# Kernel tuning notes

Hardware: AMD Instinct MI355X
Metric: run time of the kernel (lower is better)

The kernel has to match this reference:

```python
import jax, jax.numpy as jnp
import numpy as np

RATIO_THRESHOLD = 0.8  # Lowe ratio
DISTANCE_THRESHOLD = None
DO_MUTUAL_CHECK = True


def setup_inputs() -> dict:
    key = jax.random.key(0)
    k0, k1 = jax.random.split(key)
    b, d, n, m = 8, 256, 4096, 4096
    d0 = jax.random.normal(k0, (b, d, n), dtype=jnp.float32)
    d1 = jax.random.normal(k1, (b, d, m), dtype=jnp.float32)
    # L2-normalize along descriptor dim so sim is cosine similarity in [-1, 1]
    d0 = d0 / jnp.linalg.norm(d0, axis=1, keepdims=True)
    d1 = d1 / jnp.linalg.norm(d1, axis=1, keepdims=True)
    return {"descriptors0": d0, "descriptors1": d1}


def find_nn(sim, ratio_thresh, distance_thresh):
    k = 2 if ratio_thresh else 1
    sim_nn, ind_nn = jax.lax.top_k(sim, k)  # [b, n, k]
    dist_nn = 2.0 * (1.0 - sim_nn)
    mask = jnp.ones(ind_nn.shape[:-1], dtype=bool)
    if ratio_thresh:
        mask = mask & (dist_nn[..., 0] <= (ratio_thresh ** 2) * dist_nn[..., 1])
    if distance_thresh:
        mask = mask & (dist_nn[..., 0] <= distance_thresh ** 2)
    matches = jnp.where(mask, ind_nn[..., 0], -1)
    scores = jnp.where(mask, (sim_nn[..., 0] + 1.0) / 2.0, 0.0)
    return matches, scores


def mutual_check(m0, m1):
    inds0 = jnp.arange(m0.shape[-1])
    safe = jnp.where(m0 > -1, m0, 0)
    loop = jnp.take_along_axis(m1, safe, axis=-1)
    ok = (m0 > -1) & (inds0 == loop)
    return jnp.where(ok, m0, -1)


def reference(descriptors0, descriptors1):
    # sim[b, n, m] = <desc0[:, :, n], desc1[:, :, m]>
    sim = jnp.einsum("bdn,bdm->bnm", descriptors0, descriptors1)
    matches0, scores0 = find_nn(sim, RATIO_THRESHOLD, DISTANCE_THRESHOLD)
    if DO_MUTUAL_CHECK:
        matches1, _ = find_nn(jnp.swapaxes(sim, 1, 2), RATIO_THRESHOLD, DISTANCE_THRESHOLD)
        matches0 = mutual_check(matches0, matches1)
    return matches0, scores0
```

## Files before the change

kernel.cpp:

```cpp
#include <hip/hip_runtime.h>


typedef unsigned int uint;
typedef unsigned char uchar;
typedef int i32x4 __attribute__((ext_vector_type(4)));
typedef int i32x8 __attribute__((ext_vector_type(8)));
typedef float f32x4 __attribute__((ext_vector_type(4)));

constexpr int B_ = 8, D_ = 256, N_ = 4096;
constexpr int BMR = 128;
constexpr int BNT = 128;
constexpr int CSPLIT = 2;
constexpr int MT_ITERS = (N_ / CSPLIT) / BNT;


constexpr size_t SZ_PANEL = (size_t)B_ * N_ * D_;
constexpr size_t OFF_AT = 0;
constexpr size_t OFF_BT = SZ_PANEL;
constexpr size_t OFF_PR = 2 * SZ_PANEL;
constexpr size_t SZ_PR  = (size_t)4 * B_ * N_ * 8;
constexpr size_t OFF_PC = OFF_PR + SZ_PR;

__device__ __forceinline__ uchar f2e4m3(float f) {
  uint u = __float_as_uint(f);
  uint s = (u >> 24) & 0x80u;
  uint mag = u & 0x7FFFFFFFu;
  if (mag >= 0x43E00000u) return (uchar)(s | 0x7Eu);
  int e = (int)(mag >> 23) - 127;
  if (e >= -6) {
    uint m = (mag >> 20) & 7u;
    uint rem = mag & 0xFFFFFu;
    m += (rem > 0x80000u) || (rem == 0x80000u && (m & 1u));
    uint ef = (uint)(e + 7);
    if (m == 8u) { m = 0u; ef += 1u; }
    if (ef >= 16u) return (uchar)(s | 0x7Eu);
    return (uchar)(s | (ef << 3) | m);
  } else {
    int q = __float2int_rn(__uint_as_float(mag) * 512.0f);
    if (q >= 8) return (uchar)(s | 0x08u);
    return (uchar)(s | (uint)q);
  }
}

__device__ __forceinline__ void glds16(const void* g, void* l) {
  __builtin_amdgcn_global_load_lds(
      (const __attribute__((address_space(1))) void*)(uintptr_t)(g),
      (__attribute__((address_space(3))) void*)(uint32_t)(uintptr_t)(l),
      16, 0, 0);
}

__device__ __forceinline__ float packkey(float v, uint mask, uint tag) {
  return __uint_as_float((__float_as_uint(v) & mask) | tag);
}

__device__ __forceinline__ float med3f(float a, float b, float c) {
#if __has_builtin(__builtin_amdgcn_fmed3f)
  return __builtin_amdgcn_fmed3f(a, b, c);
#else
  return fmaxf(fminf(a, b), fminf(fmaxf(a, b), c));
#endif
}

__device__ __forceinline__ void top2p(float& s1, float& s2, float k0, float k1) {
  const float mid = med3f(s1, k0, k1);
  s1 = fmaxf(fmaxf(s1, k0), k1);
  s2 = fmaxf(s2, mid);
}

__device__ __forceinline__ void top2merge(float& s1, float& s2, float o1, float o2) {
  const float lo = fminf(s1, o1);
  s1 = fmaxf(s1, o1);
  s2 = fmaxf(lo, fmaxf(s2, o2));
}

__global__ __launch_bounds__(256)
void prep_kernel(const float* __restrict__ in0, const float* __restrict__ in1,
                 uchar* __restrict__ At, uchar* __restrict__ Bt)
{
  __shared__ uchar tile[128][44];
  const int bz = blockIdx.z;
  const float* src = (bz < 8) ? in0 : in1;
  uchar* dst = (bz < 8) ? At : Bt;
  const int b = bz & 7;
  const int n0 = blockIdx.x * 128;
  const int k0b = blockIdx.y * 32;
  const int t = threadIdx.x;

  const int kq = t >> 5;
  const int n4 = (t & 31) * 4;
  const float* pin = src + ((size_t)b * D_ + k0b + kq * 4) * N_ + n0 + n4;
  float4 v[4];
  #pragma unroll
  for (int j = 0; j < 4; ++j) v[j] = *(const float4*)(pin + (size_t)j * N_);
  #pragma unroll
  for (int i = 0; i < 4; ++i) {
    uchar4 o = make_uchar4(f2e4m3(((const float*)&v[0])[i]),
                           f2e4m3(((const float*)&v[1])[i]),
                           f2e4m3(((const float*)&v[2])[i]),
                           f2e4m3(((const float*)&v[3])[i]));
    *(uchar4*)&tile[n4 + i][kq * 4] = o;
  }
  __syncthreads();

  const int nl = t & 127, h = t >> 7;
  const int kg = k0b + h * 16;
  const int ks = kg >> 7, g = (kg >> 5) & 3, hh = (kg >> 4) & 1;
  const int q = (nl >> 6) & 1, r4 = (nl >> 4) & 3, i16 = nl & 15;
  i32x4 val;
  #pragma unroll
  for (int j = 0; j < 4; ++j)
    val[j] = *(const int*)&tile[nl][h * 16 + j * 4];
  uchar* po = dst + (size_t)b * (N_ * D_) + (size_t)blockIdx.x * 32768 +
              ks * 16384 + ((q * 4 + r4) * 2 + hh) * 1024 + (g * 16 + i16) * 16;
  *(i32x4*)po = val;
}

__global__ __launch_bounds__(256, 2)
void nn_pass(const uchar* __restrict__ A, const uchar* __restrict__ Bp,
             uint2* __restrict__ partR, uint2* __restrict__ partC)
{
  __shared__ uchar Bs[2][32768];

  const int t = threadIdx.x;
  const int bid = blockIdx.x;
  const int b = bid & 7;
  const int rb = (bid >> 3) & 31;
  const int cs = bid >> 8;
  const size_t bOff = (size_t)b * (N_ * D_);
  const int r0 = rb * BMR;

  const int l = t & 63, wid = t >> 6, wm = wid >> 1, wn = wid & 1;
  const int l15 = l & 15, g = l >> 4;
  const int lds0 = t * 16;

  const uchar* Aseg = A + bOff + (size_t)rb * 32768;
  const uchar* Bb = Bp + bOff + (size_t)cs * 524288;

  #pragma unroll
  for (int i = 0; i < 8; ++i)
    glds16(Bb + i * 4096 + lds0, (char*)Bs[0] + i * 4096 + lds0);

  i32x8 af[2][4];
  #pragma unroll
  for (int ks = 0; ks < 2; ++ks)
    #pragma unroll
    for (int mi = 0; mi < 4; ++mi) {
      const uchar* p = Aseg + ks * 16384 + ((wm * 4 + mi) * 2) * 1024 + l * 16;
      const i32x4 lo = *(const i32x4*)p;
      const i32x4 hi = *(const i32x4*)(p + 1024);
      af[ks][mi] = __builtin_shufflevector(lo, hi, 0, 1, 2, 3, 4, 5, 6, 7);
    }
  __syncthreads();

  const float NEG = __uint_as_float(0xFF800000u);
  float rs1[4][4], rs2[4][4];
  #pragma unroll
  for (int mi = 0; mi < 4; ++mi)
    #pragma unroll
    for (int rg = 0; rg < 4; ++rg) { rs1[mi][rg] = NEG; rs2[mi][rg] = NEG; }

  float cp1[4], cp2[4];

  #pragma unroll 1
  for (int mt = 0; mt < MT_ITERS; ++mt) {
    const char* cB = (const char*)Bs[mt & 1] + l * 16;

    if (mt + 1 < MT_ITERS) {
      const uchar* Bnx = Bb + (size_t)(mt + 1) * 32768;
      #pragma unroll
      for (int i = 0; i < 8; ++i)
        glds16(Bnx + i * 4096 + lds0, (char*)Bs[(mt + 1) & 1] + i * 4096 + lds0);
    }

    if (mt > 0 && g == 0) {
      const int cbp = (mt - 1) * BNT + wn * 64;
      #pragma unroll
      for (int ni = 0; ni < 4; ++ni)
        partC[((size_t)(rb * 2 + wm) * B_ + b) * N_ + cs * 2048 + cbp + ni * 16 + l15] =
            make_uint2(__float_as_uint(cp1[ni]), __float_as_uint(cp2[ni]));
    }

    f32x4 acc[4][4];
    #pragma unroll
    for (int mi = 0; mi < 4; ++mi)
      #pragma unroll
      for (int ni = 0; ni < 4; ++ni) acc[mi][ni] = (f32x4){0.f, 0.f, 0.f, 0.f};

    #pragma unroll
    for (int ni = 0; ni < 4; ++ni) {
      const int imm = ((wn * 4 + ni) * 2) * 1024;
      const i32x4 lo = *(const i32x4*)(cB + imm);
      const i32x4 hi = *(const i32x4*)(cB + imm + 1024);
      const i32x8 bf = __builtin_shufflevector(lo, hi, 0, 1, 2, 3, 4, 5, 6, 7);
      __builtin_amdgcn_s_setprio(1);
      #pragma unroll
      for (int mi = 0; mi < 4; ++mi)
        acc[mi][ni] = __builtin_amdgcn_mfma_scale_f32_16x16x128_f8f6f4(
            af[0][mi], bf, acc[mi][ni], 0, 0, 0, 127, 0, 127);
      __builtin_amdgcn_s_setprio(0);
    }
    #pragma unroll
    for (int ni = 0; ni < 4; ++ni) {
      const int imm = 16384 + ((wn * 4 + ni) * 2) * 1024;
      const i32x4 lo = *(const i32x4*)(cB + imm);
      const i32x4 hi = *(const i32x4*)(cB + imm + 1024);
      const i32x8 bf = __builtin_shufflevector(lo, hi, 0, 1, 2, 3, 4, 5, 6, 7);
      __builtin_amdgcn_s_setprio(1);
      #pragma unroll
      for (int mi = 0; mi < 4; ++mi)
        acc[mi][ni] = __builtin_amdgcn_mfma_scale_f32_16x16x128_f8f6f4(
            af[1][mi], bf, acc[mi][ni], 0, 0, 0, 127, 0, 127);
      __builtin_amdgcn_s_setprio(0);
    }

    const int colb = mt * BNT + wn * 64;
    const uint tg0 = (uint)(2047 - (colb + l15));
    #pragma unroll
    for (int mi = 0; mi < 4; ++mi)
      #pragma unroll
      for (int rg = 0; rg < 4; ++rg) {
        const float k0 = packkey(acc[mi][0][rg], 0xFFFFF800u, tg0);
        const float k1 = packkey(acc[mi][1][rg], 0xFFFFF800u, tg0 - 16);
        const float k2 = packkey(acc[mi][2][rg], 0xFFFFF800u, tg0 - 32);
        const float k3 = packkey(acc[mi][3][rg], 0xFFFFF800u, tg0 - 48);
        top2p(rs1[mi][rg], rs2[mi][rg], k0, k1);
        top2p(rs1[mi][rg], rs2[mi][rg], k2, k3);
      }
    const uint tgb = (uint)(63 - g * 4);
    #pragma unroll
    for (int ni = 0; ni < 4; ++ni) {
      float c1 = NEG, c2 = NEG;
      #pragma unroll
      for (int mi = 0; mi < 4; ++mi) {
        const float k0 = packkey(acc[mi][ni][0], 0xFFFFFFC0u, tgb - (uint)(mi * 16));
        const float k1 = packkey(acc[mi][ni][1], 0xFFFFFFC0u, tgb - (uint)(mi * 16 + 1));
        const float k2 = packkey(acc[mi][ni][2], 0xFFFFFFC0u, tgb - (uint)(mi * 16 + 2));
        const float k3 = packkey(acc[mi][ni][3], 0xFFFFFFC0u, tgb - (uint)(mi * 16 + 3));
        top2p(c1, c2, k0, k1);
        top2p(c1, c2, k2, k3);
      }
      #pragma unroll
      for (int off = 16; off <= 32; off <<= 1) {
        const float o1 = __shfl_xor(c1, off);
        const float o2 = __shfl_xor(c2, off);
        top2merge(c1, c2, o1, o2);
      }
      cp1[ni] = c1; cp2[ni] = c2;
    }
    __syncthreads();
  }

  if (g == 0) {
    const int cbp = (MT_ITERS - 1) * BNT + wn * 64;
    #pragma unroll
    for (int ni = 0; ni < 4; ++ni)
      partC[((size_t)(rb * 2 + wm) * B_ + b) * N_ + cs * 2048 + cbp + ni * 16 + l15] =
          make_uint2(__float_as_uint(cp1[ni]), __float_as_uint(cp2[ni]));
  }

  #pragma unroll
  for (int off = 1; off < 16; off <<= 1) {
    #pragma unroll
    for (int mi = 0; mi < 4; ++mi)
      #pragma unroll
      for (int rg = 0; rg < 4; ++rg) {
        const float o1 = __shfl_xor(rs1[mi][rg], off);
        const float o2 = __shfl_xor(rs2[mi][rg], off);
        top2merge(rs1[mi][rg], rs2[mi][rg], o1, o2);
      }
  }
  if (l15 == 0) {
    #pragma unroll
    for (int mi = 0; mi < 4; ++mi)
      #pragma unroll
      for (int rg = 0; rg < 4; ++rg)
        partR[((size_t)(cs * 2 + wn) * B_ + b) * N_ + r0 + wm * 64 + mi * 16 + g * 4 + rg] =
            make_uint2(__float_as_uint(rs1[mi][rg]), __float_as_uint(rs2[mi][rg]));
  }
}

__global__ __launch_bounds__(256)
void finalize_kernel(const uint2* __restrict__ pR, const uint2* __restrict__ pC,
                     float* __restrict__ out)
{
  const int i = blockIdx.x * 256 + threadIdx.x;
  if (i >= B_ * N_) return;
  const int b = i >> 12;
  const int n = i & (N_ - 1);
  const float NEG = __uint_as_float(0xFF800000u);

  float s1 = NEG, s2 = NEG; int bs = 0;
  #pragma unroll
  for (int sl = 0; sl < 4; ++sl) {
    const uint2 v = pR[(size_t)sl * B_ * N_ + i];
    const float o1 = __uint_as_float(v.x), o2 = __uint_as_float(v.y);
    bs = (o1 > s1) ? sl : bs;
    top2merge(s1, s2, o1, o2);
  }
  const uint k1 = __float_as_uint(s1);
  const int col = (bs >> 1) * 2048 + 2047 - (int)(k1 & 0x7FFu);
  const float v1 = __uint_as_float(k1 & 0xFFFFF800u);
  const float v2 = __uint_as_float(__float_as_uint(s2) & 0xFFFFF800u);
  const bool ok = (1.0f - v1) <= 0.64f * (1.0f - v2);

  out[B_ * N_ + i] = ok ? (v1 + 1.0f) * 0.5f : 0.0f;

  int res = -1;
  if (ok) {
    float c1 = NEG, c2 = NEG; int cbs = 0;
    const uint2* pcb = pC + (size_t)b * N_ + col;
    #pragma unroll 8
    for (int sl = 0; sl < 64; ++sl) {
      const uint2 v = pcb[(size_t)sl * B_ * N_];
      const float o1 = __uint_as_float(v.x), o2 = __uint_as_float(v.y);
      cbs = (o1 > c1) ? sl : cbs;
      top2merge(c1, c2, o1, o2);
    }
    const uint ck1 = __float_as_uint(c1);
    const int row = cbs * 64 + 63 - (int)(ck1 & 0x3Fu);
    const float cv1 = __uint_as_float(ck1 & 0xFFFFFFC0u);
    const float cv2 = __uint_as_float(__float_as_uint(c2) & 0xFFFFFFC0u);
    const bool cok = (1.0f - cv1) <= 0.64f * (1.0f - cv2);
    if (cok && row == n) res = col;
  }
  out[i] = (float)res;
}

extern "C" void kernel_launch(void* const* d_in, const int* in_sizes, int n_in,
                              void* d_out, int out_size, void* d_ws, size_t ws_size,
                              hipStream_t stream)
{
  const float* d0 = (const float*)d_in[0];
  const float* d1 = (const float*)d_in[1];
  float* out = (float*)d_out;

  uchar* At = (uchar*)((char*)d_ws + OFF_AT);
  uchar* Bt = (uchar*)((char*)d_ws + OFF_BT);
  uint2* PR = (uint2*)((char*)d_ws + OFF_PR);
  uint2* PC = (uint2*)((char*)d_ws + OFF_PC);

  prep_kernel<<<dim3(N_ / 128, D_ / 32, 16), 256, 0, stream>>>(d0, d1, At, Bt);
  nn_pass<<<dim3(B_ * (N_ / BMR) * CSPLIT), 256, 0, stream>>>(At, Bt, PR, PC);
  finalize_kernel<<<dim3(B_ * N_ / 256), 256, 0, stream>>>(PR, PC, out);
}
```

Measured before the change: 77.34 us.

## Stage B tiles through a three-slot half-tile LDS ring and buffer column partials

Replaces the two-slot, full-tile LDS double buffer with a three-slot ring of half-tiles, one per K-slice. Loads are issued further ahead, with explicit vmcnt waits and raw s_barrier calls placed between compute phases. Column top-2 partials now go to an LDS scratch buffer instead of being stored to global memory inside the main loop, and are written out with coalesced stores at the end. This aims to keep global stores out of the vmcnt accounting and to overlap B loads with MFMA work more smoothly. The cost is more LDS per block, which could limit occupancy, and four barriers per iteration instead of one.

```diff
diff --git a/kernel.cpp b/kernel.cpp
--- a/kernel.cpp
+++ b/kernel.cpp
@@ -73,6 +73,9 @@
   s2 = fmaxf(lo, fmaxf(s2, o2));
 }
 
+#define CFENCE() asm volatile("" ::: "memory")
+#define BARRIER() do { CFENCE(); __builtin_amdgcn_s_barrier(); CFENCE(); } while (0)
+
 __global__ __launch_bounds__(256)
 void prep_kernel(const float* __restrict__ in0, const float* __restrict__ in1,
                  uchar* __restrict__ At, uchar* __restrict__ Bt)
@@ -119,7 +122,8 @@
 void nn_pass(const uchar* __restrict__ A, const uchar* __restrict__ Bp,
              uint2* __restrict__ partR, uint2* __restrict__ partC)
 {
-  __shared__ uchar Bs[2][32768];
+  __shared__ uchar ring[3][16384];
+  __shared__ uint2 scrC[4096];
 
   const int t = threadIdx.x;
   const int bid = blockIdx.x;
@@ -136,10 +140,6 @@
   const uchar* Aseg = A + bOff + (size_t)rb * 32768;
   const uchar* Bb = Bp + bOff + (size_t)cs * 524288;
 
-  #pragma unroll
-  for (int i = 0; i < 8; ++i)
-    glds16(Bb + i * 4096 + lds0, (char*)Bs[0] + i * 4096 + lds0);
-
   i32x8 af[2][4];
   #pragma unroll
   for (int ks = 0; ks < 2; ++ks)
@@ -150,42 +150,17 @@
       const i32x4 hi = *(const i32x4*)(p + 1024);
       af[ks][mi] = __builtin_shufflevector(lo, hi, 0, 1, 2, 3, 4, 5, 6, 7);
     }
-  __syncthreads();
-
-  const float NEG = __uint_as_float(0xFF800000u);
-  float rs1[4][4], rs2[4][4];
-  #pragma unroll
-  for (int mi = 0; mi < 4; ++mi)
-    #pragma unroll
-    for (int rg = 0; rg < 4; ++rg) { rs1[mi][rg] = NEG; rs2[mi][rg] = NEG; }
-
-  float cp1[4], cp2[4];
-
-  #pragma unroll 1
-  for (int mt = 0; mt < MT_ITERS; ++mt) {
-    const char* cB = (const char*)Bs[mt & 1] + l * 16;
-
-    if (mt + 1 < MT_ITERS) {
-      const uchar* Bnx = Bb + (size_t)(mt + 1) * 32768;
-      #pragma unroll
-      for (int i = 0; i < 8; ++i)
-        glds16(Bnx + i * 4096 + lds0, (char*)Bs[(mt + 1) & 1] + i * 4096 + lds0);
-    }
-
-    if (mt > 0 && g == 0) {
-      const int cbp = (mt - 1) * BNT + wn * 64;
-      #pragma unroll
-      for (int ni = 0; ni < 4; ++ni)
-        partC[((size_t)(rb * 2 + wm) * B_ + b) * N_ + cs * 2048 + cbp + ni * 16 + l15] =
-            make_uint2(__float_as_uint(cp1[ni]), __float_as_uint(cp2[ni]));
-    }
-
-    f32x4 acc[4][4];
-    #pragma unroll
-    for (int mi = 0; mi < 4; ++mi)
-      #pragma unroll
-      for (int ni = 0; ni < 4; ++ni) acc[mi][ni] = (f32x4){0.f, 0.f, 0.f, 0.f};
-
+
+  auto STAGE = [&](int tile, int ksl, int slot) {
+    const uchar* src = Bb + (size_t)tile * 32768 + (size_t)ksl * 16384;
+    char* dst = (char*)ring[slot];
+    #pragma unroll
+    for (int i = 0; i < 4; ++i)
+      glds16(src + i * 4096 + lds0, dst + i * 4096 + lds0);
+  };
+
+  auto COMPUTE = [&](int slot, const i32x8 (&afk)[4], f32x4 (&acc)[4][4]) {
+    const char* cB = (const char*)ring[slot] + l * 16;
     #pragma unroll
     for (int ni = 0; ni < 4; ++ni) {
       const int imm = ((wn * 4 + ni) * 2) * 1024;
@@ -196,23 +171,19 @@
       #pragma unroll
       for (int mi = 0; mi < 4; ++mi)
         acc[mi][ni] = __builtin_amdgcn_mfma_scale_f32_16x16x128_f8f6f4(
-            af[0][mi], bf, acc[mi][ni], 0, 0, 0, 127, 0, 127);
+            afk[mi], bf, acc[mi][ni], 0, 0, 0, 127, 0, 127);
       __builtin_amdgcn_s_setprio(0);
     }
-    #pragma unroll
-    for (int ni = 0; ni < 4; ++ni) {
-      const int imm = 16384 + ((wn * 4 + ni) * 2) * 1024;
-      const i32x4 lo = *(const i32x4*)(cB + imm);
-      const i32x4 hi = *(const i32x4*)(cB + imm + 1024);
-      const i32x8 bf = __builtin_shufflevector(lo, hi, 0, 1, 2, 3, 4, 5, 6, 7);
-      __builtin_amdgcn_s_setprio(1);
-      #pragma unroll
-      for (int mi = 0; mi < 4; ++mi)
-        acc[mi][ni] = __builtin_amdgcn_mfma_scale_f32_16x16x128_f8f6f4(
-            af[1][mi], bf, acc[mi][ni], 0, 0, 0, 127, 0, 127);
-      __builtin_amdgcn_s_setprio(0);
-    }
-
+  };
+
+  const float NEG = __uint_as_float(0xFF800000u);
+  float rs1[4][4], rs2[4][4];
+  #pragma unroll
+  for (int mi = 0; mi < 4; ++mi)
+    #pragma unroll
+    for (int rg = 0; rg < 4; ++rg) { rs1[mi][rg] = NEG; rs2[mi][rg] = NEG; }
+
+  auto FOLD = [&](int mt, f32x4 (&acc)[4][4]) {
     const int colb = mt * BNT + wn * 64;
     const uint tg0 = (uint)(2047 - (colb + l15));
     #pragma unroll
@@ -245,17 +216,74 @@
         const float o2 = __shfl_xor(c2, off);
         top2merge(c1, c2, o1, o2);
       }
-      cp1[ni] = c1; cp2[ni] = c2;
+      if (g == 0)
+        scrC[(((mt * 2 + wm) * 2 + wn) * 4 + ni) * 16 + l15] =
+            make_uint2(__float_as_uint(c1), __float_as_uint(c2));
     }
-    __syncthreads();
-  }
-
-  if (g == 0) {
-    const int cbp = (MT_ITERS - 1) * BNT + wn * 64;
-    #pragma unroll
-    for (int ni = 0; ni < 4; ++ni)
-      partC[((size_t)(rb * 2 + wm) * B_ + b) * N_ + cs * 2048 + cbp + ni * 16 + l15] =
-          make_uint2(__float_as_uint(cp1[ni]), __float_as_uint(cp2[ni]));
+  };
+
+  STAGE(0, 0, 0);
+  STAGE(0, 1, 1);
+  asm volatile("s_waitcnt vmcnt(0)" ::: "memory");
+  BARRIER();
+
+  int rcur = 0;
+
+  #pragma unroll 1
+  for (int mt = 0; mt < MT_ITERS - 1; ++mt) {
+    f32x4 acc[4][4];
+    #pragma unroll
+    for (int mi = 0; mi < 4; ++mi)
+      #pragma unroll
+      for (int ni = 0; ni < 4; ++ni) acc[mi][ni] = (f32x4){0.f, 0.f, 0.f, 0.f};
+
+    int rn2 = rcur + 2; if (rn2 >= 3) rn2 -= 3;
+    int rn1 = rcur + 1; if (rn1 >= 3) rn1 -= 3;
+
+    STAGE(mt + 1, 0, rn2);
+    asm volatile("s_waitcnt vmcnt(8)" ::: "memory");
+    BARRIER();
+    COMPUTE(rcur, af[0], acc);
+    BARRIER();
+
+    STAGE(mt + 1, 1, rcur);
+    asm volatile("s_waitcnt vmcnt(8)" ::: "memory");
+    BARRIER();
+    COMPUTE(rn1, af[1], acc);
+    FOLD(mt, acc);
+    BARRIER();
+
+    rcur = rn2;
+  }
+
+  {
+    f32x4 acc[4][4];
+    #pragma unroll
+    for (int mi = 0; mi < 4; ++mi)
+      #pragma unroll
+      for (int ni = 0; ni < 4; ++ni) acc[mi][ni] = (f32x4){0.f, 0.f, 0.f, 0.f};
+    int rn1 = rcur + 1; if (rn1 >= 3) rn1 -= 3;
+
+    asm volatile("s_waitcnt vmcnt(4)" ::: "memory");
+    BARRIER();
+    COMPUTE(rcur, af[0], acc);
+    BARRIER();
+
+    asm volatile("s_waitcnt vmcnt(0)" ::: "memory");
+    BARRIER();
+    COMPUTE(rn1, af[1], acc);
+    FOLD(MT_ITERS - 1, acc);
+    BARRIER();
+  }
+
+  {
+    const int wmD = t >> 7;
+    const int cc = t & 127;
+    const uint2* sp = &scrC[(size_t)(((cc >> 3) * 2 + wmD) * 2 + ((cc >> 2) & 1)) * 64 +
+                            (cc & 3) * 16];
+    uint2* gp = partC + ((size_t)(rb * 2 + wmD) * B_ + b) * N_ + cs * 2048 + cc * 16;
+    #pragma unroll
+    for (int j = 0; j < 16; ++j) gp[j] = sp[j];
   }
 
   #pragma unroll
```

Result: no change. 77.61 us (+0.4%).

## Retile NN pass to 64-row blocks with 8 column waves and split-K staging

Applied to the files above, without the earlier changes.

Reorganizes the fused GEMM+top2 kernel: blocks now cover 64 rows with 512 threads, each of 8 waves owning a 16-column slice, and the B tile is staged in two K-halves so the next half's load overlaps the current MFMAs. Per-wave accumulators shrink from 16 to 4 vectors, cutting register pressure to allow higher occupancy, and LDS per block is halved. In exchange, A fragments are loaded twice as often across blocks, the block count doubles, there are more barriers per iteration, and partR grows to 16 slices that finalize must merge.

```diff
diff --git a/kernel.cpp b/kernel.cpp
--- a/kernel.cpp
+++ b/kernel.cpp
@@ -8,17 +8,15 @@
 typedef float f32x4 __attribute__((ext_vector_type(4)));
 
 constexpr int B_ = 8, D_ = 256, N_ = 4096;
-constexpr int BMR = 128;
-constexpr int BNT = 128;
 constexpr int CSPLIT = 2;
-constexpr int MT_ITERS = (N_ / CSPLIT) / BNT;
+constexpr int MT_ITERS = (N_ / CSPLIT) / 128;
 
 
 constexpr size_t SZ_PANEL = (size_t)B_ * N_ * D_;
 constexpr size_t OFF_AT = 0;
 constexpr size_t OFF_BT = SZ_PANEL;
 constexpr size_t OFF_PR = 2 * SZ_PANEL;
-constexpr size_t SZ_PR  = (size_t)4 * B_ * N_ * 8;
+constexpr size_t SZ_PR  = (size_t)16 * B_ * N_ * 8;
 constexpr size_t OFF_PC = OFF_PR + SZ_PR;
 
 __device__ __forceinline__ uchar f2e4m3(float f) {
@@ -61,6 +59,12 @@
 #endif
 }
 
+__device__ __forceinline__ void top2(float& s1, float& s2, float k) {
+  const float m = med3f(s1, s2, k);
+  s1 = fmaxf(s1, k);
+  s2 = m;
+}
+
 __device__ __forceinline__ void top2p(float& s1, float& s2, float k0, float k1) {
   const float mid = med3f(s1, k0, k1);
   s1 = fmaxf(fmaxf(s1, k0), k1);
@@ -115,37 +119,42 @@
   *(i32x4*)po = val;
 }
 
-__global__ __launch_bounds__(256, 2)
+__global__ __launch_bounds__(512, 4)
 void nn_pass(const uchar* __restrict__ A, const uchar* __restrict__ Bp,
              uint2* __restrict__ partR, uint2* __restrict__ partC)
 {
-  __shared__ uchar Bs[2][32768];
+  __shared__ uchar Bs[2][16384];
 
   const int t = threadIdx.x;
   const int bid = blockIdx.x;
   const int b = bid & 7;
-  const int rb = (bid >> 3) & 31;
-  const int cs = bid >> 8;
+  const int rb = (bid >> 3) & 63;
+  const int cs = bid >> 9;
   const size_t bOff = (size_t)b * (N_ * D_);
-  const int r0 = rb * BMR;
-
-  const int l = t & 63, wid = t >> 6, wm = wid >> 1, wn = wid & 1;
+  const int r0 = rb * 64;
+
+  const int l = t & 63, wn = t >> 6;
   const int l15 = l & 15, g = l >> 4;
   const int lds0 = t * 16;
 
-  const uchar* Aseg = A + bOff + (size_t)rb * 32768;
+  const uchar* Apan = A + bOff + (size_t)(rb >> 1) * 32768;
+  const int q = rb & 1;
   const uchar* Bb = Bp + bOff + (size_t)cs * 524288;
 
-  #pragma unroll
-  for (int i = 0; i < 8; ++i)
-    glds16(Bb + i * 4096 + lds0, (char*)Bs[0] + i * 4096 + lds0);
-
+  auto STAGE = [&](int tile, int ksl, int slot) {
+    const uchar* src = Bb + (size_t)tile * 32768 + (size_t)ksl * 16384;
+    #pragma unroll
+    for (int i = 0; i < 2; ++i)
+      glds16(src + i * 8192 + lds0, (char*)Bs[slot] + i * 8192 + lds0);
+  };
+
+  STAGE(0, 0, 0);
   i32x8 af[2][4];
   #pragma unroll
   for (int ks = 0; ks < 2; ++ks)
     #pragma unroll
     for (int mi = 0; mi < 4; ++mi) {
-      const uchar* p = Aseg + ks * 16384 + ((wm * 4 + mi) * 2) * 1024 + l * 16;
+      const uchar* p = Apan + ks * 16384 + ((q * 4 + mi) * 2) * 1024 + l * 16;
       const i32x4 lo = *(const i32x4*)p;
       const i32x4 hi = *(const i32x4*)(p + 1024);
       af[ks][mi] = __builtin_shufflevector(lo, hi, 0, 1, 2, 3, 4, 5, 6, 7);
@@ -159,83 +168,63 @@
     #pragma unroll
     for (int rg = 0; rg < 4; ++rg) { rs1[mi][rg] = NEG; rs2[mi][rg] = NEG; }
 
-  float cp1[4], cp2[4];
+  float cp1 = NEG, cp2 = NEG;
 
   #pragma unroll 1
   for (int mt = 0; mt < MT_ITERS; ++mt) {
-    const char* cB = (const char*)Bs[mt & 1] + l * 16;
-
-    if (mt + 1 < MT_ITERS) {
-      const uchar* Bnx = Bb + (size_t)(mt + 1) * 32768;
-      #pragma unroll
-      for (int i = 0; i < 8; ++i)
-        glds16(Bnx + i * 4096 + lds0, (char*)Bs[(mt + 1) & 1] + i * 4096 + lds0);
-    }
-
-    if (mt > 0 && g == 0) {
-      const int cbp = (mt - 1) * BNT + wn * 64;
-      #pragma unroll
-      for (int ni = 0; ni < 4; ++ni)
-        partC[((size_t)(rb * 2 + wm) * B_ + b) * N_ + cs * 2048 + cbp + ni * 16 + l15] =
-            make_uint2(__float_as_uint(cp1[ni]), __float_as_uint(cp2[ni]));
-    }
-
-    f32x4 acc[4][4];
-    #pragma unroll
-    for (int mi = 0; mi < 4; ++mi)
-      #pragma unroll
-      for (int ni = 0; ni < 4; ++ni) acc[mi][ni] = (f32x4){0.f, 0.f, 0.f, 0.f};
-
-    #pragma unroll
-    for (int ni = 0; ni < 4; ++ni) {
-      const int imm = ((wn * 4 + ni) * 2) * 1024;
-      const i32x4 lo = *(const i32x4*)(cB + imm);
-      const i32x4 hi = *(const i32x4*)(cB + imm + 1024);
+    if (mt > 0 && g == 0)
+      partC[((size_t)rb * B_ + b) * N_ + cs * 2048 + (mt - 1) * 128 + wn * 16 + l15] =
+          make_uint2(__float_as_uint(cp1), __float_as_uint(cp2));
+
+    f32x4 acc[4];
+    #pragma unroll
+    for (int mi = 0; mi < 4; ++mi) acc[mi] = (f32x4){0.f, 0.f, 0.f, 0.f};
+
+    STAGE(mt, 1, 1);
+    {
+      const char* cB = (const char*)Bs[0] + wn * 2048 + l * 16;
+      const i32x4 lo = *(const i32x4*)cB;
+      const i32x4 hi = *(const i32x4*)(cB + 1024);
       const i32x8 bf = __builtin_shufflevector(lo, hi, 0, 1, 2, 3, 4, 5, 6, 7);
       __builtin_amdgcn_s_setprio(1);
       #pragma unroll
       for (int mi = 0; mi < 4; ++mi)
-        acc[mi][ni] = __builtin_amdgcn_mfma_scale_f32_16x16x128_f8f6f4(
-            af[0][mi], bf, acc[mi][ni], 0, 0, 0, 127, 0, 127);
+        acc[mi] = __builtin_amdgcn_mfma_scale_f32_16x16x128_f8f6f4(
+            af[0][mi], bf, acc[mi], 0, 0, 0, 127, 0, 127);
       __builtin_amdgcn_s_setprio(0);
     }
-    #pragma unroll
-    for (int ni = 0; ni < 4; ++ni) {
-      const int imm = 16384 + ((wn * 4 + ni) * 2) * 1024;
-      const i32x4 lo = *(const i32x4*)(cB + imm);
-      const i32x4 hi = *(const i32x4*)(cB + imm + 1024);
+    __syncthreads();
+
+    if (mt + 1 < MT_ITERS) STAGE(mt + 1, 0, 0);
+    {
+      const char* cB = (const char*)Bs[1] + wn * 2048 + l * 16;
+      const i32x4 lo = *(const i32x4*)cB;
+      const i32x4 hi = *(const i32x4*)(cB + 1024);
       const i32x8 bf = __builtin_shufflevector(lo, hi, 0, 1, 2, 3, 4, 5, 6, 7);
       __builtin_amdgcn_s_setprio(1);
       #pragma unroll
       for (int mi = 0; mi < 4; ++mi)
-        acc[mi][ni] = __builtin_amdgcn_mfma_scale_f32_16x16x128_f8f6f4(
-            af[1][mi], bf, acc[mi][ni], 0, 0, 0, 127, 0, 127);
+        acc[mi] = __builtin_amdgcn_mfma_scale_f32_16x16x128_f8f6f4(
+            af[1][mi], bf, acc[mi], 0, 0, 0, 127, 0, 127);
       __builtin_amdgcn_s_setprio(0);
     }
 
-    const int colb = mt * BNT + wn * 64;
-    const uint tg0 = (uint)(2047 - (colb + l15));
+    const uint tagc = (uint)(2047 - (mt * 128 + wn * 16 + l15));
     #pragma unroll
     for (int mi = 0; mi < 4; ++mi)
       #pragma unroll
-      for (int rg = 0; rg < 4; ++rg) {
-        const float k0 = packkey(acc[mi][0][rg], 0xFFFFF800u, tg0);
-        const float k1 = packkey(acc[mi][1][rg], 0xFFFFF800u, tg0 - 16);
-        const float k2 = packkey(acc[mi][2][rg], 0xFFFFF800u, tg0 - 32);
-        const float k3 = packkey(acc[mi][3][rg], 0xFFFFF800u, tg0 - 48);
-        top2p(rs1[mi][rg], rs2[mi][rg], k0, k1);
-        top2p(rs1[mi][rg], rs2[mi][rg], k2, k3);
-      }
-    const uint tgb = (uint)(63 - g * 4);
-    #pragma unroll
-    for (int ni = 0; ni < 4; ++ni) {
+      for (int rg = 0; rg < 4; ++rg)
+        top2(rs1[mi][rg], rs2[mi][rg], packkey(acc[mi][rg], 0xFFFFF800u, tagc));
+
+    {
+      const uint tgb = (uint)(63 - g * 4);
       float c1 = NEG, c2 = NEG;
       #pragma unroll
       for (int mi = 0; mi < 4; ++mi) {
-        const float k0 = packkey(acc[mi][ni][0], 0xFFFFFFC0u, tgb - (uint)(mi * 16));
-        const float k1 = packkey(acc[mi][ni][1], 0xFFFFFFC0u, tgb - (uint)(mi * 16 + 1));
-        const float k2 = packkey(acc[mi][ni][2], 0xFFFFFFC0u, tgb - (uint)(mi * 16 + 2));
-        const float k3 = packkey(acc[mi][ni][3], 0xFFFFFFC0u, tgb - (uint)(mi * 16 + 3));
+        const float k0 = packkey(acc[mi][0], 0xFFFFFFC0u, tgb - (uint)(mi * 16));
+        const float k1 = packkey(acc[mi][1], 0xFFFFFFC0u, tgb - (uint)(mi * 16 + 1));
+        const float k2 = packkey(acc[mi][2], 0xFFFFFFC0u, tgb - (uint)(mi * 16 + 2));
+        const float k3 = packkey(acc[mi][3], 0xFFFFFFC0u, tgb - (uint)(mi * 16 + 3));
         top2p(c1, c2, k0, k1);
         top2p(c1, c2, k2, k3);
       }
@@ -245,18 +234,14 @@
         const float o2 = __shfl_xor(c2, off);
         top2merge(c1, c2, o1, o2);
       }
-      cp1[ni] = c1; cp2[ni] = c2;
+      cp1 = c1; cp2 = c2;
     }
     __syncthreads();
   }
 
-  if (g == 0) {
-    const int cbp = (MT_ITERS - 1) * BNT + wn * 64;
-    #pragma unroll
-    for (int ni = 0; ni < 4; ++ni)
-      partC[((size_t)(rb * 2 + wm) * B_ + b) * N_ + cs * 2048 + cbp + ni * 16 + l15] =
-          make_uint2(__float_as_uint(cp1[ni]), __float_as_uint(cp2[ni]));
-  }
+  if (g == 0)
+    partC[((size_t)rb * B_ + b) * N_ + cs * 2048 + (MT_ITERS - 1) * 128 + wn * 16 + l15] =
+        make_uint2(__float_as_uint(cp1), __float_as_uint(cp2));
 
   #pragma unroll
   for (int off = 1; off < 16; off <<= 1) {
@@ -274,7 +259,7 @@
     for (int mi = 0; mi < 4; ++mi)
       #pragma unroll
       for (int rg = 0; rg < 4; ++rg)
-        partR[((size_t)(cs * 2 + wn) * B_ + b) * N_ + r0 + wm * 64 + mi * 16 + g * 4 + rg] =
+        partR[((size_t)(cs * 8 + wn) * B_ + b) * N_ + r0 + mi * 16 + g * 4 + rg] =
             make_uint2(__float_as_uint(rs1[mi][rg]), __float_as_uint(rs2[mi][rg]));
   }
 }
@@ -291,14 +276,14 @@
 
   float s1 = NEG, s2 = NEG; int bs = 0;
   #pragma unroll
-  for (int sl = 0; sl < 4; ++sl) {
+  for (int sl = 0; sl < 16; ++sl) {
     const uint2 v = pR[(size_t)sl * B_ * N_ + i];
     const float o1 = __uint_as_float(v.x), o2 = __uint_as_float(v.y);
     bs = (o1 > s1) ? sl : bs;
     top2merge(s1, s2, o1, o2);
   }
   const uint k1 = __float_as_uint(s1);
-  const int col = (bs >> 1) * 2048 + 2047 - (int)(k1 & 0x7FFu);
+  const int col = (bs >> 3) * 2048 + 2047 - (int)(k1 & 0x7FFu);
   const float v1 = __uint_as_float(k1 & 0xFFFFF800u);
   const float v2 = __uint_as_float(__float_as_uint(s2) & 0xFFFFF800u);
   const bool ok = (1.0f - v1) <= 0.64f * (1.0f - v2);
@@ -340,6 +325,6 @@
   uint2* PC = (uint2*)((char*)d_ws + OFF_PC);
 
   prep_kernel<<<dim3(N_ / 128, D_ / 32, 16), 256, 0, stream>>>(d0, d1, At, Bt);
-  nn_pass<<<dim3(B_ * (N_ / BMR) * CSPLIT), 256, 0, stream>>>(At, Bt, PR, PC);
+  nn_pass<<<dim3(B_ * 64 * CSPLIT), 512, 0, stream>>>(At, Bt, PR, PC);
   finalize_kernel<<<dim3(B_ * N_ / 256), 256, 0, stream>>>(PR, PC, out);
 }
```

After: 168.4 us. 118% more time.

## Load B fragments directly from global into registers, dropping LDS staging

Applied to the files above, without the earlier changes.

The prep kernel now writes the fp8 panels so each lane's 32-byte MFMA operand is contiguous, which allows single i32x8 global loads. The nn_pass kernel drops the double-buffered LDS tile, the global_load_lds copies and the per-tile barriers. B fragments are prefetched straight into registers, with the next tile's first half loaded while the current tile's MFMAs run. The goal is to remove LDS traffic and synchronisation, at the cost of higher VGPR pressure and each wave reading B from L2/global without sharing across waves.

```diff
diff --git a/kernel.cpp b/kernel.cpp
--- a/kernel.cpp
+++ b/kernel.cpp
@@ -8,10 +8,8 @@
 typedef float f32x4 __attribute__((ext_vector_type(4)));
 
 constexpr int B_ = 8, D_ = 256, N_ = 4096;
-constexpr int BMR = 128;
-constexpr int BNT = 128;
 constexpr int CSPLIT = 2;
-constexpr int MT_ITERS = (N_ / CSPLIT) / BNT;
+constexpr int MT_ITERS = (N_ / CSPLIT) / 128;
 
 
 constexpr size_t SZ_PANEL = (size_t)B_ * N_ * D_;
@@ -42,13 +40,6 @@
   }
 }
 
-__device__ __forceinline__ void glds16(const void* g, void* l) {
-  __builtin_amdgcn_global_load_lds(
-      (const __attribute__((address_space(1))) void*)(uintptr_t)(g),
-      (__attribute__((address_space(3))) void*)(uint32_t)(uintptr_t)(l),
-      16, 0, 0);
-}
-
 __device__ __forceinline__ float packkey(float v, uint mask, uint tag) {
   return __uint_as_float((__float_as_uint(v) & mask) | tag);
 }
@@ -105,13 +96,14 @@
   const int nl = t & 127, h = t >> 7;
   const int kg = k0b + h * 16;
   const int ks = kg >> 7, g = (kg >> 5) & 3, hh = (kg >> 4) & 1;
-  const int q = (nl >> 6) & 1, r4 = (nl >> 4) & 3, i16 = nl & 15;
+  const int f = ((nl >> 6) & 1) * 4 + ((nl >> 4) & 3);
+  const int l = g * 16 + (nl & 15);
   i32x4 val;
   #pragma unroll
   for (int j = 0; j < 4; ++j)
     val[j] = *(const int*)&tile[nl][h * 16 + j * 4];
   uchar* po = dst + (size_t)b * (N_ * D_) + (size_t)blockIdx.x * 32768 +
-              ks * 16384 + ((q * 4 + r4) * 2 + hh) * 1024 + (g * 16 + i16) * 16;
+              ks * 16384 + f * 2048 + l * 32 + hh * 16;
   *(i32x4*)po = val;
 }
 
@@ -119,38 +111,26 @@
 void nn_pass(const uchar* __restrict__ A, const uchar* __restrict__ Bp,
              uint2* __restrict__ partR, uint2* __restrict__ partC)
 {
-  __shared__ uchar Bs[2][32768];
-
   const int t = threadIdx.x;
   const int bid = blockIdx.x;
   const int b = bid & 7;
   const int rb = (bid >> 3) & 31;
   const int cs = bid >> 8;
   const size_t bOff = (size_t)b * (N_ * D_);
-  const int r0 = rb * BMR;
+  const int r0 = rb * 128;
 
   const int l = t & 63, wid = t >> 6, wm = wid >> 1, wn = wid & 1;
   const int l15 = l & 15, g = l >> 4;
-  const int lds0 = t * 16;
 
   const uchar* Aseg = A + bOff + (size_t)rb * 32768;
   const uchar* Bb = Bp + bOff + (size_t)cs * 524288;
 
-  #pragma unroll
-  for (int i = 0; i < 8; ++i)
-    glds16(Bb + i * 4096 + lds0, (char*)Bs[0] + i * 4096 + lds0);
-
-  i32x8 af[2][4];
-  #pragma unroll
-  for (int ks = 0; ks < 2; ++ks)
-    #pragma unroll
-    for (int mi = 0; mi < 4; ++mi) {
-      const uchar* p = Aseg + ks * 16384 + ((wm * 4 + mi) * 2) * 1024 + l * 16;
-      const i32x4 lo = *(const i32x4*)p;
-      const i32x4 hi = *(const i32x4*)(p + 1024);
-      af[ks][mi] = __builtin_shufflevector(lo, hi, 0, 1, 2, 3, 4, 5, 6, 7);
-    }
-  __syncthreads();
+  i32x8 af0[4], af1[4];
+  #pragma unroll
+  for (int mi = 0; mi < 4; ++mi) {
+    af0[mi] = *(const i32x8*)(Aseg +         (wm * 4 + mi) * 2048 + l * 32);
+    af1[mi] = *(const i32x8*)(Aseg + 16384 + (wm * 4 + mi) * 2048 + l * 32);
+  }
 
   const float NEG = __uint_as_float(0xFF800000u);
   float rs1[4][4], rs2[4][4];
@@ -159,61 +139,26 @@
     #pragma unroll
     for (int rg = 0; rg < 4; ++rg) { rs1[mi][rg] = NEG; rs2[mi][rg] = NEG; }
 
-  float cp1[4], cp2[4];
-
-  #pragma unroll 1
-  for (int mt = 0; mt < MT_ITERS; ++mt) {
-    const char* cB = (const char*)Bs[mt & 1] + l * 16;
-
-    if (mt + 1 < MT_ITERS) {
-      const uchar* Bnx = Bb + (size_t)(mt + 1) * 32768;
-      #pragma unroll
-      for (int i = 0; i < 8; ++i)
-        glds16(Bnx + i * 4096 + lds0, (char*)Bs[(mt + 1) & 1] + i * 4096 + lds0);
-    }
-
-    if (mt > 0 && g == 0) {
-      const int cbp = (mt - 1) * BNT + wn * 64;
-      #pragma unroll
-      for (int ni = 0; ni < 4; ++ni)
-        partC[((size_t)(rb * 2 + wm) * B_ + b) * N_ + cs * 2048 + cbp + ni * 16 + l15] =
-            make_uint2(__float_as_uint(cp1[ni]), __float_as_uint(cp2[ni]));
-    }
-
-    f32x4 acc[4][4];
-    #pragma unroll
-    for (int mi = 0; mi < 4; ++mi)
-      #pragma unroll
-      for (int ni = 0; ni < 4; ++ni) acc[mi][ni] = (f32x4){0.f, 0.f, 0.f, 0.f};
-
-    #pragma unroll
-    for (int ni = 0; ni < 4; ++ni) {
-      const int imm = ((wn * 4 + ni) * 2) * 1024;
-      const i32x4 lo = *(const i32x4*)(cB + imm);
-      const i32x4 hi = *(const i32x4*)(cB + imm + 1024);
-      const i32x8 bf = __builtin_shufflevector(lo, hi, 0, 1, 2, 3, 4, 5, 6, 7);
-      __builtin_amdgcn_s_setprio(1);
+  auto LOADB = [&](i32x8 (&dst)[4], int mt, int ks) {
+    const uchar* p = Bb + (size_t)mt * 32768 + ks * 16384 + wn * 8192 + l * 32;
+    #pragma unroll
+    for (int ni = 0; ni < 4; ++ni)
+      dst[ni] = *(const i32x8*)(p + ni * 2048);
+  };
+
+  auto MFMAH = [&](const i32x8 (&afk)[4], const i32x8 (&bf)[4], f32x4 (&acc)[4][4]) {
+    __builtin_amdgcn_s_setprio(1);
+    #pragma unroll
+    for (int ni = 0; ni < 4; ++ni)
       #pragma unroll
       for (int mi = 0; mi < 4; ++mi)
         acc[mi][ni] = __builtin_amdgcn_mfma_scale_f32_16x16x128_f8f6f4(
-            af[0][mi], bf, acc[mi][ni], 0, 0, 0, 127, 0, 127);
-      __builtin_amdgcn_s_setprio(0);
-    }
-    #pragma unroll
-    for (int ni = 0; ni < 4; ++ni) {
-      const int imm = 16384 + ((wn * 4 + ni) * 2) * 1024;
-      const i32x4 lo = *(const i32x4*)(cB + imm);
-      const i32x4 hi = *(const i32x4*)(cB + imm + 1024);
-      const i32x8 bf = __builtin_shufflevector(lo, hi, 0, 1, 2, 3, 4, 5, 6, 7);
-      __builtin_amdgcn_s_setprio(1);
-      #pragma unroll
-      for (int mi = 0; mi < 4; ++mi)
-        acc[mi][ni] = __builtin_amdgcn_mfma_scale_f32_16x16x128_f8f6f4(
-            af[1][mi], bf, acc[mi][ni], 0, 0, 0, 127, 0, 127);
-      __builtin_amdgcn_s_setprio(0);
-    }
-
-    const int colb = mt * BNT + wn * 64;
+            afk[mi], bf[ni], acc[mi][ni], 0, 0, 0, 127, 0, 127);
+    __builtin_amdgcn_s_setprio(0);
+  };
+
+  auto FOLD = [&](int mt, f32x4 (&acc)[4][4]) {
+    const int colb = mt * 128 + wn * 64;
     const uint tg0 = (uint)(2047 - (colb + l15));
     #pragma unroll
     for (int mi = 0; mi < 4; ++mi)
@@ -245,17 +190,33 @@
         const float o2 = __shfl_xor(c2, off);
         top2merge(c1, c2, o1, o2);
       }
-      cp1[ni] = c1; cp2[ni] = c2;
+      if (g == 0)
+        partC[((size_t)(rb * 2 + wm) * B_ + b) * N_ + cs * 2048 + colb + ni * 16 + l15] =
+            make_uint2(__float_as_uint(c1), __float_as_uint(c2));
     }
-    __syncthreads();
-  }
-
-  if (g == 0) {
-    const int cbp = (MT_ITERS - 1) * BNT + wn * 64;
-    #pragma unroll
-    for (int ni = 0; ni < 4; ++ni)
-      partC[((size_t)(rb * 2 + wm) * B_ + b) * N_ + cs * 2048 + cbp + ni * 16 + l15] =
-          make_uint2(__float_as_uint(cp1[ni]), __float_as_uint(cp2[ni]));
+  };
+
+  auto TILE = [&](int mt, i32x8 (&pf)[4], i32x8 (&nx)[4]) {
+    f32x4 acc[4][4];
+    #pragma unroll
+    for (int mi = 0; mi < 4; ++mi)
+      #pragma unroll
+      for (int ni = 0; ni < 4; ++ni) acc[mi][ni] = (f32x4){0.f, 0.f, 0.f, 0.f};
+    i32x8 b1[4];
+    LOADB(b1, mt, 1);
+    MFMAH(af0, pf, acc);
+    LOADB(nx, (mt + 1) & 15, 0);
+    MFMAH(af1, b1, acc);
+    FOLD(mt, acc);
+  };
+
+  i32x8 pfA[4], pfB[4];
+  LOADB(pfA, 0, 0);
+
+  #pragma unroll 1
+  for (int mt = 0; mt < MT_ITERS; mt += 2) {
+    TILE(mt,     pfA, pfB);
+    TILE(mt + 1, pfB, pfA);
   }
 
   #pragma unroll
@@ -340,6 +301,6 @@
   uint2* PC = (uint2*)((char*)d_ws + OFF_PC);
 
   prep_kernel<<<dim3(N_ / 128, D_ / 32, 16), 256, 0, stream>>>(d0, d1, At, Bt);
-  nn_pass<<<dim3(B_ * (N_ / BMR) * CSPLIT), 256, 0, stream>>>(At, Bt, PR, PC);
+  nn_pass<<<dim3(B_ * 32 * CSPLIT), 256, 0, stream>>>(At, Bt, PR, PC);
   finalize_kernel<<<dim3(B_ * N_ / 256), 256, 0, stream>>>(PR, PC, out);
 }
```

Result: slower. 137.1 us (+77.3%).
